# Kernel tuning notes

Measured on AMD Instinct MI355X. Metric: run time of the kernel, lower is better.

## Reference

```python
import jax, jax.numpy as jnp
import numpy as np

HEADS = 16
NEG = -1e9  # matches masked_fill(-1000000000.0)

def setup_inputs() -> dict:
    key = jax.random.key(0)
    ks = jax.random.split(key, 7)
    B, T, C = 2, 2048, 1024
    s = 1.0 / np.sqrt(C)
    return {
        "q": jax.random.normal(ks[0], (B, T, C), jnp.float32),
        "k": jax.random.normal(ks[1], (B, T, C), jnp.float32),
        "v": jax.random.normal(ks[2], (B, T, C), jnp.float32),
        "Wq": jax.random.normal(ks[3], (C, C), jnp.float32) * s,
        "Wk": jax.random.normal(ks[4], (C, C), jnp.float32) * s,
        "Wv": jax.random.normal(ks[5], (C, C), jnp.float32) * s,
        "Wo": jax.random.normal(ks[6], (C, C), jnp.float32) * s,
    }

def reference(q, k, v, Wq, Wk, Wv, Wo):
    B, T, C = q.shape
    h = HEADS
    dk = C // h
    # torch Linear (no bias): y = x @ W.T ; weight is [out, in]
    def proj(x, W):
        return (x @ W.T).reshape(B, T, h, dk).transpose(0, 2, 1, 3)  # [B,h,T,dk]
    qh, kh, vh = proj(q, Wq), proj(k, Wk), proj(v, Wv)
    scale = jnp.asarray(dk, q.dtype) ** 0.5
    scores = jnp.einsum('bhqd,bhkd->bhqk', qh / scale, kh)  # [B,h,T,T]
    causal = jnp.tril(jnp.ones((T, T), dtype=bool))
    scores = jnp.where(causal[None, None], scores, jnp.asarray(NEG, scores.dtype))
    attn = jax.nn.softmax(scores, axis=-1)
    out = jnp.einsum('bhqk,bhkd->bhqd', attn, vh)  # [B,h,T,dk]
    concat = out.transpose(0, 2, 1, 3).reshape(B, T, C)
    return concat @ Wo.T
```

## Files before the change

kernel.cpp:

```cpp
#include <hip/hip_runtime.h>
#include <hip/hip_bf16.h>

typedef __bf16 bf16x8 __attribute__((ext_vector_type(8)));
typedef float  f32x4  __attribute__((ext_vector_type(4)));
typedef unsigned short u16;

__device__ __forceinline__ u16 f2bf(float f) {
    __bf16 h = (__bf16)f;
    return __builtin_bit_cast(u16, h);
}

__device__ __forceinline__ f32x4 mfma16(bf16x8 a, bf16x8 b, f32x4 c) {
    return __builtin_amdgcn_mfma_f32_16x16x32_bf16(a, b, c, 0, 0, 0);
}

__global__ __launch_bounds__(256) void cvtW(const float* __restrict__ W0,
                                            const float* __restrict__ W1,
                                            const float* __restrict__ W2,
                                            const float* __restrict__ W3,
                                            u16* __restrict__ dst) {
    const int t     = blockIdx.x * 256 + threadIdx.x;
    const int which = t >> 17;
    const int off   = (t & 0x1FFFF) * 8;
    const float* s  = (which == 0) ? W0 : (which == 1) ? W1 : (which == 2) ? W2 : W3;
    float4 f0 = *(const float4*)(s + off);
    float4 f1 = *(const float4*)(s + off + 4);
    bf16x8 u;
    u[0] = (__bf16)f0.x; u[1] = (__bf16)f0.y; u[2] = (__bf16)f0.z; u[3] = (__bf16)f0.w;
    u[4] = (__bf16)f1.x; u[5] = (__bf16)f1.y; u[6] = (__bf16)f1.z; u[7] = (__bf16)f1.w;
    *(bf16x8*)(dst + ((size_t)which << 20) + off) = u;
}

__global__ __launch_bounds__(256) void gemm_qkv(const float* __restrict__ q,
                                                const float* __restrict__ k,
                                                const float* __restrict__ v,
                                                const u16* __restrict__ Wb,
                                                u16* __restrict__ Qp,
                                                u16* __restrict__ Kp,
                                                u16* __restrict__ Vt) {
    constexpr int K = 1024, N = 1024;
    __shared__ __align__(16) u16 As[128 * 32];
    __shared__ __align__(16) u16 Bs[128 * 32];

    const int tid  = threadIdx.x;
    const int lane = tid & 63;
    const int w    = tid >> 6;
    const int wr = w >> 1, wc = w & 1;
    const int wg    = (blockIdx.x & 7) * 96 + (blockIdx.x >> 3);
    const int which = wg >> 8;
    const int inner = wg & 255;
    const int m0 = (inner >> 3) * 128, n0 = (inner & 7) * 128;
    const int colg = lane & 15, rowg = lane >> 4;

    const float* A = (which == 0) ? q : (which == 1) ? k : v;
    const u16*   W = Wb + ((size_t)which << 20);

    size_t aoff[2], boff[2];
    int wio[2];
#pragma unroll
    for (int i = 0; i < 2; ++i) {
        const int c   = i * 256 + tid;
        const int row = c >> 2;
        const int kc  = c & 3;
        aoff[i] = (size_t)(m0 + row) * K + kc * 8;
        boff[i] = (size_t)(n0 + row) * K + kc * 8;
        const int kcs = kc ^ ((row >> 1) & 3);
        wio[i] = row * 32 + kcs * 8;
    }
    const int kcr  = rowg ^ ((colg >> 1) & 3);
    const int rbase = colg * 32 + kcr * 8;

    f32x4 acc[4][4];
#pragma unroll
    for (int i = 0; i < 4; ++i)
#pragma unroll
        for (int j = 0; j < 4; ++j) acc[i][j] = (f32x4){0.f, 0.f, 0.f, 0.f};

    for (int t = 0; t < 32; ++t) {
        const int kk = t * 32;
        float4 a0[2], a1[2];
        uint4  bv[2];
#pragma unroll
        for (int i = 0; i < 2; ++i) {
            a0[i] = *(const float4*)(A + aoff[i] + kk);
            a1[i] = *(const float4*)(A + aoff[i] + kk + 4);
            bv[i] = *(const uint4*)(W + boff[i] + kk);
        }
#pragma unroll
        for (int i = 0; i < 2; ++i) {
            bf16x8 u;
            u[0] = (__bf16)a0[i].x; u[1] = (__bf16)a0[i].y;
            u[2] = (__bf16)a0[i].z; u[3] = (__bf16)a0[i].w;
            u[4] = (__bf16)a1[i].x; u[5] = (__bf16)a1[i].y;
            u[6] = (__bf16)a1[i].z; u[7] = (__bf16)a1[i].w;
            *(bf16x8*)(&As[wio[i]]) = u;
            *(uint4*)(&Bs[wio[i]]) = bv[i];
        }
        __syncthreads();

        bf16x8 af[4], bfr[4];
#pragma unroll
        for (int mi = 0; mi < 4; ++mi)
            af[mi] = *(const bf16x8*)(&As[(wr * 64 + mi * 16) * 32 + rbase]);
#pragma unroll
        for (int ni = 0; ni < 4; ++ni)
            bfr[ni] = *(const bf16x8*)(&Bs[(wc * 64 + ni * 16) * 32 + rbase]);
#pragma unroll
        for (int mi = 0; mi < 4; ++mi)
#pragma unroll
            for (int ni = 0; ni < 4; ++ni)
                acc[mi][ni] = mfma16(af[mi], bfr[ni], acc[mi][ni]);
        __syncthreads();
    }

    u16* Crm = (which == 0) ? Qp : Kp;
#pragma unroll
    for (int mi = 0; mi < 4; ++mi) {
#pragma unroll
        for (int ni = 0; ni < 4; ++ni) {
#pragma unroll
            for (int r = 0; r < 4; ++r) {
                const int row = m0 + wr * 64 + mi * 16 + rowg * 4 + r;
                const int col = n0 + wc * 64 + ni * 16 + colg;
                const float vv = acc[mi][ni][r];
                if (which < 2) {
                    Crm[(size_t)row * N + col] = f2bf(vv);
                } else {
                    const int b = row >> 11, tt = row & 2047;
                    const int h = col >> 6,  d = col & 63;
                    Vt[((size_t)((b * 16 + h) * 64 + d) << 11) + tt] = f2bf(vv);
                }
            }
        }
    }
}

__global__ __launch_bounds__(256) void gemm_out(const u16* __restrict__ Ap,
                                                const u16* __restrict__ W,
                                                float* __restrict__ Cp) {
    constexpr int K = 1024, N = 1024;
    __shared__ __align__(16) u16 As[64 * 32];
    __shared__ __align__(16) u16 Bs[128 * 32];

    const int tid  = threadIdx.x;
    const int lane = tid & 63;
    const int w    = tid >> 6;
    const int wr = w >> 1, wc = w & 1;
    const int wg = (blockIdx.x & 7) * 64 + (blockIdx.x >> 3);
    const int m0 = (wg >> 3) * 64, n0 = (wg & 7) * 128;
    const int colg = lane & 15, rowg = lane >> 4;

    const int rowA = tid >> 2, kcA = tid & 3;
    const size_t aoff = (size_t)(m0 + rowA) * K + kcA * 8;
    const int wiA = rowA * 32 + (kcA ^ ((rowA >> 1) & 3)) * 8;

    size_t boff[2];
    int wiB[2];
#pragma unroll
    for (int i = 0; i < 2; ++i) {
        const int c   = i * 256 + tid;
        const int row = c >> 2;
        const int kc  = c & 3;
        boff[i] = (size_t)(n0 + row) * K + kc * 8;
        wiB[i] = row * 32 + (kc ^ ((row >> 1) & 3)) * 8;
    }
    const int kcr   = rowg ^ ((colg >> 1) & 3);
    const int rbase = colg * 32 + kcr * 8;

    f32x4 acc[2][4];
#pragma unroll
    for (int i = 0; i < 2; ++i)
#pragma unroll
        for (int j = 0; j < 4; ++j) acc[i][j] = (f32x4){0.f, 0.f, 0.f, 0.f};

    for (int t = 0; t < 32; ++t) {
        const int kk = t * 32;
        uint4 av = *(const uint4*)(Ap + aoff + kk);
        uint4 bv[2];
#pragma unroll
        for (int i = 0; i < 2; ++i) bv[i] = *(const uint4*)(W + boff[i] + kk);
        *(uint4*)(&As[wiA]) = av;
#pragma unroll
        for (int i = 0; i < 2; ++i) *(uint4*)(&Bs[wiB[i]]) = bv[i];
        __syncthreads();

        bf16x8 af[2], bfr[4];
#pragma unroll
        for (int mi = 0; mi < 2; ++mi)
            af[mi] = *(const bf16x8*)(&As[(wr * 32 + mi * 16) * 32 + rbase]);
#pragma unroll
        for (int ni = 0; ni < 4; ++ni)
            bfr[ni] = *(const bf16x8*)(&Bs[(wc * 64 + ni * 16) * 32 + rbase]);
#pragma unroll
        for (int mi = 0; mi < 2; ++mi)
#pragma unroll
            for (int ni = 0; ni < 4; ++ni)
                acc[mi][ni] = mfma16(af[mi], bfr[ni], acc[mi][ni]);
        __syncthreads();
    }

#pragma unroll
    for (int mi = 0; mi < 2; ++mi)
#pragma unroll
        for (int ni = 0; ni < 4; ++ni)
#pragma unroll
            for (int r = 0; r < 4; ++r) {
                const int row = m0 + wr * 32 + mi * 16 + rowg * 4 + r;
                const int col = n0 + wc * 64 + ni * 16 + colg;
                Cp[(size_t)row * N + col] = acc[mi][ni][r];
            }
}

constexpr float CEXP = 0.18033688011112042f;

__global__ __launch_bounds__(256) void attn_causal(const u16* __restrict__ Qp,
                                                   const u16* __restrict__ Kp,
                                                   const u16* __restrict__ Vt,
                                                   u16* __restrict__ concat) {
    constexpr int T = 2048, C = 1024;
    __shared__ __align__(16) u16 Ks[128 * 64];
    __shared__ __align__(16) u16 Vs[64 * 128];
    __shared__ __align__(16) u16 Pl[4][2048];

    const int tid  = threadIdx.x;
    const int lane = tid & 63;
    const int w    = tid >> 6;
    const int colg = lane & 15, rowg = lane >> 4;

    const int idx = blockIdx.x;
    const int xcd = idx & 7;
    const int i1  = idx >> 3;
    const int bh  = xcd * 4 + (i1 & 3);
    const int qg  = 31 - (i1 >> 2);
    const int b = bh >> 4, h = bh & 15;

    const int q0 = (qg * 4 + w) * 16;
    const int nt    = (q0 + 143) >> 7;
    const int ktmax = ((qg * 4 + 3) * 16 + 143) >> 7;

    const char* Kg = (const char*)(Kp + (size_t)(b * T) * C + h * 64);
    const char* Vg = (const char*)(Vt + ((size_t)(b * 16 + h) * 64) * T);
    char* Ksb = (char*)Ks;
    char* Vsb = (char*)Vs;
    char* Pw  = (char*)&Pl[w][0];

    const u16* Qb = Qp + (size_t)(b * T + q0 + colg) * C + h * 64;
    const bf16x8 qf0 = *(const bf16x8*)(Qb + rowg * 8);
    const bf16x8 qf1 = *(const bf16x8*)(Qb + 32 + rowg * 8);

    float mm = -1e30f, ll = 0.f;
    f32x4 O[4];
#pragma unroll
    for (int g = 0; g < 4; ++g) O[g] = (f32x4){0.f, 0.f, 0.f, 0.f};

    const int sw = (colg & 7) << 4;

    for (int kt = 0; kt < ktmax; ++kt) {
        const int kvb = kt * 128;
        uint4 kst[4], vst[4];
#pragma unroll
        for (int i2 = 0; i2 < 4; ++i2) {
            const int s  = i2 * 4096 + tid * 16;
            const int kv = s >> 7, ir = s & 127;
            kst[i2] = *(const uint4*)(Kg + (size_t)(kvb + kv) * 2048 + ir);
            const int d = s >> 8, irv = s & 255;
            vst[i2] = *(const uint4*)(Vg + (size_t)d * 4096 + (size_t)kvb * 2 + irv);
        }
#pragma unroll
        for (int i2 = 0; i2 < 4; ++i2) {
            const int s  = i2 * 4096 + tid * 16;
            const int kv = s >> 7;
            *(uint4*)(Ksb + (s ^ ((kv & 7) << 4))) = kst[i2];
            const int d = s >> 8;
            *(uint4*)(Vsb + (s ^ ((d & 7) << 4))) = vst[i2];
        }
        __syncthreads();

        if (kt < nt) {
            float pr[8][4];
#pragma unroll
            for (int sub = 0; sub < 8; ++sub) {
                const int kb = (sub * 16 + colg) * 128 + rowg * 16;
                bf16x8 kf0 = *(const bf16x8*)(Ksb + (kb ^ sw));
                bf16x8 kf1 = *(const bf16x8*)(Ksb + ((kb + 64) ^ sw));
                f32x4 t = (f32x4){0.f, 0.f, 0.f, 0.f};
                t = mfma16(kf0, qf0, t);
                t = mfma16(kf1, qf1, t);
#pragma unroll
                for (int r = 0; r < 4; ++r) pr[sub][r] = t[r];
            }
            if (kvb + 127 > q0) {
#pragma unroll
                for (int sub = 0; sub < 8; ++sub)
#pragma unroll
                    for (int r = 0; r < 4; ++r)
                        if (kvb + sub * 16 + rowg * 4 + r > q0 + colg) pr[sub][r] = -1e30f;
            }
            float mx[8];
#pragma unroll
            for (int sub = 0; sub < 8; ++sub)
                mx[sub] = fmaxf(fmaxf(pr[sub][0], pr[sub][1]), fmaxf(pr[sub][2], pr[sub][3]));
            float pm = fmaxf(fmaxf(fmaxf(mx[0], mx[1]), fmaxf(mx[2], mx[3])),
                             fmaxf(fmaxf(mx[4], mx[5]), fmaxf(mx[6], mx[7])));
            pm = fmaxf(pm, __shfl_xor(pm, 16, 64));
            pm = fmaxf(pm, __shfl_xor(pm, 32, 64));
            if (__any(pm > mm + 40.f)) {
                const float mn = fmaxf(mm, pm);
                const float sc = __builtin_amdgcn_exp2f((mm - mn) * CEXP);
                mm = mn;
                ll *= sc;
#pragma unroll
                for (int r = 0; r < 4; ++r) {
                    const float scr = __shfl(sc, (lane & 48) + rowg * 4 + r, 64);
#pragma unroll
                    for (int g = 0; g < 4; ++g) O[g][r] *= scr;
                }
            }
            float rs = 0.f;
#pragma unroll
            for (int sub = 0; sub < 8; ++sub) {
                const float e0 = __builtin_amdgcn_exp2f((pr[sub][0] - mm) * CEXP);
                const float e1 = __builtin_amdgcn_exp2f((pr[sub][1] - mm) * CEXP);
                const float e2 = __builtin_amdgcn_exp2f((pr[sub][2] - mm) * CEXP);
                const float e3 = __builtin_amdgcn_exp2f((pr[sub][3] - mm) * CEXP);
                pr[sub][0] = e0; pr[sub][1] = e1; pr[sub][2] = e2; pr[sub][3] = e3;
                rs += (e0 + e1) + (e2 + e3);
            }
            rs += __shfl_xor(rs, 16, 64);
            rs += __shfl_xor(rs, 32, 64);
            ll += rs;
#pragma unroll
            for (int sub = 0; sub < 8; ++sub) {
                uint2 pk;
                pk.x = (unsigned)f2bf(pr[sub][0]) | ((unsigned)f2bf(pr[sub][1]) << 16);
                pk.y = (unsigned)f2bf(pr[sub][2]) | ((unsigned)f2bf(pr[sub][3]) << 16);
                const int wb = (colg * 256 + sub * 32 + rowg * 8) ^ sw;
                *(uint2*)(Pw + wb) = pk;
            }
            bf16x8 pf[4];
#pragma unroll
            for (int kc = 0; kc < 4; ++kc)
                pf[kc] = *(const bf16x8*)(Pw + ((colg * 256 + kc * 64 + rowg * 16) ^ sw));
#pragma unroll
            for (int g = 0; g < 4; ++g) {
                const int vb0 = (g * 16 + colg) * 256 + rowg * 16;
#pragma unroll
                for (int kc = 0; kc < 4; ++kc) {
                    bf16x8 vf = *(const bf16x8*)(Vsb + ((vb0 + kc * 64) ^ sw));
                    O[g] = mfma16(pf[kc], vf, O[g]);
                }
            }
        }
        __syncthreads();
    }

#pragma unroll
    for (int r = 0; r < 4; ++r) {
        const float lr = __shfl(ll, (lane & 48) + rowg * 4 + r, 64);
        const float rc = 1.f / lr;
        const size_t base = (size_t)(b * T + q0 + rowg * 4 + r) * C + h * 64;
#pragma unroll
        for (int g = 0; g < 4; ++g)
            concat[base + g * 16 + colg] = f2bf(O[g][r] * rc);
    }
}

extern "C" void kernel_launch(void* const* d_in, const int* in_sizes, int n_in,
                              void* d_out, int out_size, void* d_ws, size_t ws_size,
                              hipStream_t stream) {
    const float* q  = (const float*)d_in[0];
    const float* k  = (const float*)d_in[1];
    const float* v  = (const float*)d_in[2];
    const float* Wq = (const float*)d_in[3];
    const float* Wk = (const float*)d_in[4];
    const float* Wv = (const float*)d_in[5];
    const float* Wo = (const float*)d_in[6];
    float* out = (float*)d_out;

    constexpr size_t NELEM = (size_t)4096 * 1024;
    constexpr size_t WSZ   = (size_t)1 << 20;
    u16* Wbf = (u16*)d_ws;
    u16* Qp  = Wbf + 4 * WSZ;
    u16* Kp  = Qp + NELEM;
    u16* Vt  = Kp + NELEM;
    u16* Cc  = Vt + NELEM;

    cvtW<<<2048, 256, 0, stream>>>(Wq, Wk, Wv, Wo, Wbf);

    gemm_qkv<<<768, 256, 0, stream>>>(q, k, v, Wbf, Qp, Kp, Vt);

    attn_causal<<<1024, 256, 0, stream>>>(Qp, Kp, Vt, Cc);

    gemm_out<<<512, 256, 0, stream>>>(Cc, Wbf + 3 * WSZ, out);
}
```

Before: 138.0 us.

## Double-buffer LDS tiles in QKV and output projection GEMMs

Both projection GEMMs now use two shared-memory buffers. The next K-tile's global loads are issued before the MFMA work on the current tile and written to the alternate buffer afterward, so each iteration needs one barrier instead of two. This aims to hide global-memory latency behind matrix math, at the cost of twice the LDS and more live registers holding prefetched data. A small helper for float-to-bf16 packing is also factored out.

```diff
diff --git a/kernel.cpp b/kernel.cpp
--- a/kernel.cpp
+++ b/kernel.cpp
@@ -12,6 +12,13 @@
 
 __device__ __forceinline__ f32x4 mfma16(bf16x8 a, bf16x8 b, f32x4 c) {
     return __builtin_amdgcn_mfma_f32_16x16x32_bf16(a, b, c, 0, 0, 0);
+}
+
+__device__ __forceinline__ bf16x8 cvt8(float4 a0, float4 a1) {
+    bf16x8 u;
+    u[0] = (__bf16)a0.x; u[1] = (__bf16)a0.y; u[2] = (__bf16)a0.z; u[3] = (__bf16)a0.w;
+    u[4] = (__bf16)a1.x; u[5] = (__bf16)a1.y; u[6] = (__bf16)a1.z; u[7] = (__bf16)a1.w;
+    return u;
 }
 
 __global__ __launch_bounds__(256) void cvtW(const float* __restrict__ W0,
@@ -25,10 +32,7 @@
     const float* s  = (which == 0) ? W0 : (which == 1) ? W1 : (which == 2) ? W2 : W3;
     float4 f0 = *(const float4*)(s + off);
     float4 f1 = *(const float4*)(s + off + 4);
-    bf16x8 u;
-    u[0] = (__bf16)f0.x; u[1] = (__bf16)f0.y; u[2] = (__bf16)f0.z; u[3] = (__bf16)f0.w;
-    u[4] = (__bf16)f1.x; u[5] = (__bf16)f1.y; u[6] = (__bf16)f1.z; u[7] = (__bf16)f1.w;
-    *(bf16x8*)(dst + ((size_t)which << 20) + off) = u;
+    *(bf16x8*)(dst + ((size_t)which << 20) + off) = cvt8(f0, f1);
 }
 
 __global__ __launch_bounds__(256) void gemm_qkv(const float* __restrict__ q,
@@ -39,8 +43,8 @@
                                                 u16* __restrict__ Kp,
                                                 u16* __restrict__ Vt) {
     constexpr int K = 1024, N = 1024;
-    __shared__ __align__(16) u16 As[128 * 32];
-    __shared__ __align__(16) u16 Bs[128 * 32];
+    __shared__ __align__(16) u16 As[2][4096];
+    __shared__ __align__(16) u16 Bs[2][4096];
 
     const int tid  = threadIdx.x;
     const int lane = tid & 63;
@@ -67,7 +71,7 @@
         const int kcs = kc ^ ((row >> 1) & 3);
         wio[i] = row * 32 + kcs * 8;
     }
-    const int kcr  = rowg ^ ((colg >> 1) & 3);
+    const int kcr   = rowg ^ ((colg >> 1) & 3);
     const int rbase = colg * 32 + kcr * 8;
 
     f32x4 acc[4][4];
@@ -76,41 +80,55 @@
 #pragma unroll
         for (int j = 0; j < 4; ++j) acc[i][j] = (f32x4){0.f, 0.f, 0.f, 0.f};
 
+    float4 a0[2], a1[2];
+    uint4  bv[2];
+#pragma unroll
+    for (int i = 0; i < 2; ++i) {
+        a0[i] = *(const float4*)(A + aoff[i]);
+        a1[i] = *(const float4*)(A + aoff[i] + 4);
+        bv[i] = *(const uint4*)(W + boff[i]);
+    }
+#pragma unroll
+    for (int i = 0; i < 2; ++i) {
+        *(bf16x8*)(&As[0][wio[i]]) = cvt8(a0[i], a1[i]);
+        *(uint4*)(&Bs[0][wio[i]]) = bv[i];
+    }
+    __syncthreads();
+
+    int p = 0;
     for (int t = 0; t < 32; ++t) {
-        const int kk = t * 32;
-        float4 a0[2], a1[2];
-        uint4  bv[2];
-#pragma unroll
-        for (int i = 0; i < 2; ++i) {
-            a0[i] = *(const float4*)(A + aoff[i] + kk);
-            a1[i] = *(const float4*)(A + aoff[i] + kk + 4);
-            bv[i] = *(const uint4*)(W + boff[i] + kk);
-        }
-#pragma unroll
-        for (int i = 0; i < 2; ++i) {
-            bf16x8 u;
-            u[0] = (__bf16)a0[i].x; u[1] = (__bf16)a0[i].y;
-            u[2] = (__bf16)a0[i].z; u[3] = (__bf16)a0[i].w;
-            u[4] = (__bf16)a1[i].x; u[5] = (__bf16)a1[i].y;
-            u[6] = (__bf16)a1[i].z; u[7] = (__bf16)a1[i].w;
-            *(bf16x8*)(&As[wio[i]]) = u;
-            *(uint4*)(&Bs[wio[i]]) = bv[i];
+        if (t < 31) {
+            const int kk = (t + 1) * 32;
+#pragma unroll
+            for (int i = 0; i < 2; ++i) {
+                a0[i] = *(const float4*)(A + aoff[i] + kk);
+                a1[i] = *(const float4*)(A + aoff[i] + kk + 4);
+                bv[i] = *(const uint4*)(W + boff[i] + kk);
+            }
+        }
+        {
+            bf16x8 af[4], bfr[4];
+#pragma unroll
+            for (int mi = 0; mi < 4; ++mi)
+                af[mi] = *(const bf16x8*)(&As[p][(wr * 64 + mi * 16) * 32 + rbase]);
+#pragma unroll
+            for (int ni = 0; ni < 4; ++ni)
+                bfr[ni] = *(const bf16x8*)(&Bs[p][(wc * 64 + ni * 16) * 32 + rbase]);
+#pragma unroll
+            for (int mi = 0; mi < 4; ++mi)
+#pragma unroll
+                for (int ni = 0; ni < 4; ++ni)
+                    acc[mi][ni] = mfma16(af[mi], bfr[ni], acc[mi][ni]);
+        }
+        if (t < 31) {
+#pragma unroll
+            for (int i = 0; i < 2; ++i) {
+                *(bf16x8*)(&As[p ^ 1][wio[i]]) = cvt8(a0[i], a1[i]);
+                *(uint4*)(&Bs[p ^ 1][wio[i]]) = bv[i];
+            }
         }
         __syncthreads();
-
-        bf16x8 af[4], bfr[4];
-#pragma unroll
-        for (int mi = 0; mi < 4; ++mi)
-            af[mi] = *(const bf16x8*)(&As[(wr * 64 + mi * 16) * 32 + rbase]);
-#pragma unroll
-        for (int ni = 0; ni < 4; ++ni)
-            bfr[ni] = *(const bf16x8*)(&Bs[(wc * 64 + ni * 16) * 32 + rbase]);
-#pragma unroll
-        for (int mi = 0; mi < 4; ++mi)
-#pragma unroll
-            for (int ni = 0; ni < 4; ++ni)
-                acc[mi][ni] = mfma16(af[mi], bfr[ni], acc[mi][ni]);
-        __syncthreads();
+        p ^= 1;
     }
 
     u16* Crm = (which == 0) ? Qp : Kp;
@@ -139,8 +157,8 @@
                                                 const u16* __restrict__ W,
                                                 float* __restrict__ Cp) {
     constexpr int K = 1024, N = 1024;
-    __shared__ __align__(16) u16 As[64 * 32];
-    __shared__ __align__(16) u16 Bs[128 * 32];
+    __shared__ __align__(16) u16 As[2][2048];
+    __shared__ __align__(16) u16 Bs[2][4096];
 
     const int tid  = threadIdx.x;
     const int lane = tid & 63;
@@ -173,30 +191,44 @@
 #pragma unroll
         for (int j = 0; j < 4; ++j) acc[i][j] = (f32x4){0.f, 0.f, 0.f, 0.f};
 
+    uint4 av = *(const uint4*)(Ap + aoff);
+    uint4 bv[2];
+#pragma unroll
+    for (int i = 0; i < 2; ++i) bv[i] = *(const uint4*)(W + boff[i]);
+    *(uint4*)(&As[0][wiA]) = av;
+#pragma unroll
+    for (int i = 0; i < 2; ++i) *(uint4*)(&Bs[0][wiB[i]]) = bv[i];
+    __syncthreads();
+
+    int p = 0;
     for (int t = 0; t < 32; ++t) {
-        const int kk = t * 32;
-        uint4 av = *(const uint4*)(Ap + aoff + kk);
-        uint4 bv[2];
-#pragma unroll
-        for (int i = 0; i < 2; ++i) bv[i] = *(const uint4*)(W + boff[i] + kk);
-        *(uint4*)(&As[wiA]) = av;
-#pragma unroll
-        for (int i = 0; i < 2; ++i) *(uint4*)(&Bs[wiB[i]]) = bv[i];
+        if (t < 31) {
+            const int kk = (t + 1) * 32;
+            av = *(const uint4*)(Ap + aoff + kk);
+#pragma unroll
+            for (int i = 0; i < 2; ++i) bv[i] = *(const uint4*)(W + boff[i] + kk);
+        }
+        {
+            bf16x8 af[2], bfr[4];
+#pragma unroll
+            for (int mi = 0; mi < 2; ++mi)
+                af[mi] = *(const bf16x8*)(&As[p][(wr * 32 + mi * 16) * 32 + rbase]);
+#pragma unroll
+            for (int ni = 0; ni < 4; ++ni)
+                bfr[ni] = *(const bf16x8*)(&Bs[p][(wc * 64 + ni * 16) * 32 + rbase]);
+#pragma unroll
+            for (int mi = 0; mi < 2; ++mi)
+#pragma unroll
+                for (int ni = 0; ni < 4; ++ni)
+                    acc[mi][ni] = mfma16(af[mi], bfr[ni], acc[mi][ni]);
+        }
+        if (t < 31) {
+            *(uint4*)(&As[p ^ 1][wiA]) = av;
+#pragma unroll
+            for (int i = 0; i < 2; ++i) *(uint4*)(&Bs[p ^ 1][wiB[i]]) = bv[i];
+        }
         __syncthreads();
-
-        bf16x8 af[2], bfr[4];
-#pragma unroll
-        for (int mi = 0; mi < 2; ++mi)
-            af[mi] = *(const bf16x8*)(&As[(wr * 32 + mi * 16) * 32 + rbase]);
-#pragma unroll
-        for (int ni = 0; ni < 4; ++ni)
-            bfr[ni] = *(const bf16x8*)(&Bs[(wc * 64 + ni * 16) * 32 + rbase]);
-#pragma unroll
-        for (int mi = 0; mi < 2; ++mi)
-#pragma unroll
-            for (int ni = 0; ni < 4; ++ni)
-                acc[mi][ni] = mfma16(af[mi], bfr[ni], acc[mi][ni]);
-        __syncthreads();
+        p ^= 1;
     }
 
 #pragma unroll
```

Result: faster. 134.4 us (-2.6%).
